# Performance work log

Hardware: AMD Instinct MI355X
Metric: run time of the kernel (lower is better)

The kernel has to match this reference:

```python
import math
import jax, jax.numpy as jnp
import numpy as np

GRID = (256, 256, 256)
K = 9                # kernel_size (already odd)
SIGMA = K / 4.0
PAD = K // 2
CLIP = 0.03


def _gaussian_kernel():
    ax = np.arange(K, dtype=np.float32)
    mean = (K - 1) / 2.0
    g = np.exp(-(((ax - mean) / SIGMA) ** 2) / 2.0) / (SIGMA * math.sqrt(2.0 * math.pi))
    k = g[:, None, None] * g[None, :, None] * g[None, None, :]
    k = k / k.sum()
    return jnp.asarray(k, dtype=jnp.float32).reshape(1, 1, K, K, K)  # OIDHW


def setup_inputs() -> dict:
    key = jax.random.key(0)
    x = jax.random.normal(key, (int(np.prod(GRID)),), dtype=jnp.float32)
    kernel = _gaussian_kernel()
    return {"x": x, "kernel": kernel}


def reference(x, kernel):
    v = x.reshape(1, 1, *GRID)  # [1,1,D,H,W]
    # reflect padding (torch padding_mode='reflect', padding = K//2)
    p = jnp.pad(v, ((0, 0), (0, 0), (PAD, PAD), (PAD, PAD), (PAD, PAD)), mode="reflect")
    # torch Conv3d is cross-correlation; lax conv does not flip kernels either
    out = jax.lax.conv_general_dilated(
        p, kernel,
        window_strides=(1, 1, 1),
        padding="VALID",
        dimension_numbers=("NCDHW", "OIDHW", "NCDHW"),
    )
    # clip: keep smoothed output within +/-CLIP of the original input
    out = jnp.maximum(jnp.minimum(v, out + CLIP), out - CLIP)
    return out.reshape(-1)
```

## Files before the change

kernel.cpp:

```cpp
#include <hip/hip_runtime.h>
#include <hip/hip_fp16.h>
#include <math.h>

#define CLIPV 0.03f

struct W9 { float g[9]; };
struct half4 { __half2 a, b; };

__device__ __forceinline__ int reflect_idx(int i, int n) {
    if (i < 0) i = -i;
    if (i >= n) i = 2 * n - 2 - i;
    return i;
}

__device__ __forceinline__ float4 h4_to_f4(half4 v) {
    const float2 ab = __half22float2(v.a), cd = __half22float2(v.b);
    float4 r; r.x = ab.x; r.y = ab.y; r.z = cd.x; r.w = cd.y; return r;
}
__device__ __forceinline__ half4 f4_to_h4(float4 v) {
    half4 r; r.a = __floats2half2_rn(v.x, v.y); r.b = __floats2half2_rn(v.z, v.w);
    return r;
}

__global__ __launch_bounds__(256, 4) void wh_pass(const float* __restrict__ x,
                                                  __half* __restrict__ t2, W9 wt) {
    const int bid = blockIdx.x;
    const int xcd = bid & 7;
    const int k   = bid >> 3;
    const int z   = xcd * 32 + (k >> 2);
    const int wv  = threadIdx.x >> 6;
    const int h0  = ((k & 3) * 4 + wv) * 16;
    const int L   = threadIdx.x & 63;
    const int w4  = L * 4;
    const bool l0 = (L == 0), l63 = (L == 63);
    const int offL = l0 ? 1 : (w4 - 4);
    const int offR = l63 ? 251 : (w4 + 4);

    const float* plane  = x  + (size_t)z * 65536;
    __half*      oplane = t2 + (size_t)z * 65536;

    float4 ring[9];

    float4 cLf, cCf, cRf, nLf, nCf, nRf;
    {
        const float* r0 = plane + (size_t)reflect_idx(h0 - 4, 256) * 256;
        cLf = *(const float4*)(r0 + offL);
        cCf = *(const float4*)(r0 + w4);
        cRf = *(const float4*)(r0 + offR);
        const float* r1 = plane + (size_t)reflect_idx(h0 - 3, 256) * 256;
        nLf = *(const float4*)(r1 + offL);
        nCf = *(const float4*)(r1 + w4);
        nRf = *(const float4*)(r1 + offR);
    }

    #pragma unroll
    for (int i = 0; i < 24; ++i) {
        float4 mLf, mCf, mRf;
        if (i < 22) {
            const float* row = plane + (size_t)reflect_idx(h0 - 2 + i, 256) * 256;
            mLf = *(const float4*)(row + offL);
            mCf = *(const float4*)(row + w4);
            mRf = *(const float4*)(row + offR);
        }

        float sv[12];
        sv[0] = l0 ? cLf.w : cLf.x;
        sv[1] = l0 ? cLf.z : cLf.y;
        sv[2] = l0 ? cLf.y : cLf.z;
        sv[3] = l0 ? cLf.x : cLf.w;
        sv[4] = cCf.x; sv[5] = cCf.y; sv[6] = cCf.z; sv[7] = cCf.w;
        sv[8]  = l63 ? cRf.w : cRf.x;
        sv[9]  = l63 ? cRf.z : cRf.y;
        sv[10] = l63 ? cRf.y : cRf.z;
        sv[11] = l63 ? cRf.x : cRf.w;

        {
            float a0 = 0.f, a1 = 0.f, a2 = 0.f, a3 = 0.f;
            #pragma unroll
            for (int j = 0; j < 9; ++j) {
                a0 = fmaf(wt.g[j], sv[j],     a0);
                a1 = fmaf(wt.g[j], sv[j + 1], a1);
                a2 = fmaf(wt.g[j], sv[j + 2], a2);
                a3 = fmaf(wt.g[j], sv[j + 3], a3);
            }
            float4 wc; wc.x = a0; wc.y = a1; wc.z = a2; wc.w = a3;
            ring[i % 9] = wc;
        }

        if (i >= 8) {
            float a0 = 0.f, a1 = 0.f, a2 = 0.f, a3 = 0.f;
            #pragma unroll
            for (int j = 0; j < 9; ++j) {
                const float4 v = ring[(i - 8 + j) % 9];
                a0 = fmaf(wt.g[j], v.x, a0);
                a1 = fmaf(wt.g[j], v.y, a1);
                a2 = fmaf(wt.g[j], v.z, a2);
                a3 = fmaf(wt.g[j], v.w, a3);
            }
            float4 o; o.x = a0; o.y = a1; o.z = a2; o.w = a3;
            *(half4*)(oplane + (size_t)(h0 + i - 8) * 256 + w4) = f4_to_h4(o);
        }

        cLf = nLf; cCf = nCf; cRf = nRf;
        nLf = mLf; nCf = mCf; nRf = mRf;
    }
}

__global__ __launch_bounds__(256) void d_clip_pass(const __half* __restrict__ t2,
                                                   const float* __restrict__ x,
                                                   float* __restrict__ out, W9 wt) {
    const int bid   = blockIdx.x;
    const int xcd   = bid & 7;
    const int k     = bid >> 3;
    const int chunk = xcd * 2 + (k & 1);
    const int tile  = k >> 1;
    const int z0    = chunk * 16;
    const size_t c4 = (size_t)tile * 256 + threadIdx.x;

    const half4*  t4 = (const half4*)t2;
    const float4* xp = (const float4*)x;
    float4*       o4 = (float4*)out;

    float4 ring[9];

    half4 cur = t4[(size_t)reflect_idx(z0 - 4, 256) * 16384 + c4];
    half4 nxt = t4[(size_t)reflect_idx(z0 - 3, 256) * 16384 + c4];
    float4 xCur, xNxt;

    #pragma unroll
    for (int i = 0; i < 24; ++i) {
        half4 nn;
        if (i < 22)
            nn = t4[(size_t)reflect_idx(z0 - 2 + i, 256) * 16384 + c4];
        float4 xNew;
        if (i >= 6 && i < 22)
            xNew = xp[(size_t)(z0 + i - 6) * 16384 + c4];

        ring[i % 9] = h4_to_f4(cur);

        if (i >= 8) {
            const int z = z0 + i - 8;
            float a0 = 0.f, a1 = 0.f, a2 = 0.f, a3 = 0.f;
            #pragma unroll
            for (int j = 0; j < 9; ++j) {
                const float4 v = ring[(i - 8 + j) % 9];
                a0 = fmaf(wt.g[j], v.x, a0);
                a1 = fmaf(wt.g[j], v.y, a1);
                a2 = fmaf(wt.g[j], v.z, a2);
                a3 = fmaf(wt.g[j], v.w, a3);
            }
            const float4 xv = xCur;
            float4 r;
            r.x = fmaxf(fminf(xv.x, a0 + CLIPV), a0 - CLIPV);
            r.y = fmaxf(fminf(xv.y, a1 + CLIPV), a1 - CLIPV);
            r.z = fmaxf(fminf(xv.z, a2 + CLIPV), a2 - CLIPV);
            r.w = fmaxf(fminf(xv.w, a3 + CLIPV), a3 - CLIPV);
            o4[(size_t)z * 16384 + c4] = r;
        }

        cur = nxt; nxt = nn;
        xCur = xNxt; xNxt = xNew;
    }
}

extern "C" void kernel_launch(void* const* d_in, const int* in_sizes, int n_in,
                              void* d_out, int out_size, void* d_ws, size_t ws_size,
                              hipStream_t stream) {
    const float* x = (const float*)d_in[0];
    float* out = (float*)d_out;
    __half* t2 = (__half*)d_ws;

    W9 wt;
    {
        double g[9], s = 0.0;
        const double sigma = 9.0 / 4.0;
        for (int i = 0; i < 9; ++i) {
            double tt = (i - 4.0) / sigma;
            g[i] = exp(-0.5 * tt * tt);
            s += g[i];
        }
        for (int i = 0; i < 9; ++i) wt.g[i] = (float)(g[i] / s);
    }

    wh_pass<<<dim3(1024), dim3(256), 0, stream>>>(x, t2, wt);
    d_clip_pass<<<dim3(1024), dim3(256), 0, stream>>>(t2, x, out, wt);
}
```

Measured before the change: 52.75 us.

## Split fused W/H separable pass into separate H and W kernels

After: 76.10 us. +44.3%, slower.

```diff
diff --git a/kernel.cpp b/kernel.cpp
--- a/kernel.cpp
+++ b/kernel.cpp
@@ -22,70 +22,31 @@
     return r;
 }
 
-__global__ __launch_bounds__(256, 4) void wh_pass(const float* __restrict__ x,
-                                                  __half* __restrict__ t2, W9 wt) {
+__global__ __launch_bounds__(256) void h_pass(const float* __restrict__ x,
+                                              __half* __restrict__ t1, W9 wt) {
     const int bid = blockIdx.x;
     const int xcd = bid & 7;
     const int k   = bid >> 3;
     const int z   = xcd * 32 + (k >> 2);
     const int wv  = threadIdx.x >> 6;
     const int h0  = ((k & 3) * 4 + wv) * 16;
-    const int L   = threadIdx.x & 63;
-    const int w4  = L * 4;
-    const bool l0 = (L == 0), l63 = (L == 63);
-    const int offL = l0 ? 1 : (w4 - 4);
-    const int offR = l63 ? 251 : (w4 + 4);
+    const int w4  = (threadIdx.x & 63) * 4;
 
     const float* plane  = x  + (size_t)z * 65536;
-    __half*      oplane = t2 + (size_t)z * 65536;
+    __half*      oplane = t1 + (size_t)z * 65536;
 
     float4 ring[9];
 
-    float4 cLf, cCf, cRf, nLf, nCf, nRf;
-    {
-        const float* r0 = plane + (size_t)reflect_idx(h0 - 4, 256) * 256;
-        cLf = *(const float4*)(r0 + offL);
-        cCf = *(const float4*)(r0 + w4);
-        cRf = *(const float4*)(r0 + offR);
-        const float* r1 = plane + (size_t)reflect_idx(h0 - 3, 256) * 256;
-        nLf = *(const float4*)(r1 + offL);
-        nCf = *(const float4*)(r1 + w4);
-        nRf = *(const float4*)(r1 + offR);
-    }
+    float4 cur = *(const float4*)(plane + (size_t)reflect_idx(h0 - 4, 256) * 256 + w4);
+    float4 nxt = *(const float4*)(plane + (size_t)reflect_idx(h0 - 3, 256) * 256 + w4);
 
     #pragma unroll
     for (int i = 0; i < 24; ++i) {
-        float4 mLf, mCf, mRf;
-        if (i < 22) {
-            const float* row = plane + (size_t)reflect_idx(h0 - 2 + i, 256) * 256;
-            mLf = *(const float4*)(row + offL);
-            mCf = *(const float4*)(row + w4);
-            mRf = *(const float4*)(row + offR);
-        }
-
-        float sv[12];
-        sv[0] = l0 ? cLf.w : cLf.x;
-        sv[1] = l0 ? cLf.z : cLf.y;
-        sv[2] = l0 ? cLf.y : cLf.z;
-        sv[3] = l0 ? cLf.x : cLf.w;
-        sv[4] = cCf.x; sv[5] = cCf.y; sv[6] = cCf.z; sv[7] = cCf.w;
-        sv[8]  = l63 ? cRf.w : cRf.x;
-        sv[9]  = l63 ? cRf.z : cRf.y;
-        sv[10] = l63 ? cRf.y : cRf.z;
-        sv[11] = l63 ? cRf.x : cRf.w;
-
-        {
-            float a0 = 0.f, a1 = 0.f, a2 = 0.f, a3 = 0.f;
-            #pragma unroll
-            for (int j = 0; j < 9; ++j) {
-                a0 = fmaf(wt.g[j], sv[j],     a0);
-                a1 = fmaf(wt.g[j], sv[j + 1], a1);
-                a2 = fmaf(wt.g[j], sv[j + 2], a2);
-                a3 = fmaf(wt.g[j], sv[j + 3], a3);
-            }
-            float4 wc; wc.x = a0; wc.y = a1; wc.z = a2; wc.w = a3;
-            ring[i % 9] = wc;
-        }
+        float4 nn;
+        if (i < 22)
+            nn = *(const float4*)(plane + (size_t)reflect_idx(h0 - 2 + i, 256) * 256 + w4);
+
+        ring[i % 9] = cur;
 
         if (i >= 8) {
             float a0 = 0.f, a1 = 0.f, a2 = 0.f, a3 = 0.f;
@@ -101,8 +62,74 @@
             *(half4*)(oplane + (size_t)(h0 + i - 8) * 256 + w4) = f4_to_h4(o);
         }
 
-        cLf = nLf; cCf = nCf; cRf = nRf;
-        nLf = mLf; nCf = mCf; nRf = mRf;
+        cur = nxt; nxt = nn;
+    }
+}
+
+__global__ __launch_bounds__(256) void wt_pass(const __half* __restrict__ t1,
+                                               __half* __restrict__ t2, W9 wt) {
+    const int bid  = blockIdx.x;
+    const int xcd  = bid & 7;
+    const int k    = bid >> 3;
+    const int z    = xcd * 32 + (k >> 2);
+    const int band = (k & 3) * 64;
+    const int wv   = threadIdx.x >> 6;
+    const int c0   = wv * 64;
+    const int L    = threadIdx.x & 63;
+    const int r    = band + L;
+
+    const __half* row  = t1 + (size_t)z * 65536 + (size_t)r * 256;
+    __half*       orow = t2 + (size_t)z * 65536 + (size_t)r * 256;
+
+    const bool wL = (c0 == 0), wR = (c0 == 192);
+
+    float4 w0, w1, w2;
+    half4 p1, p2;
+    if (wL) {
+        w1 = h4_to_f4(*(const half4*)(row + 0));
+        w2 = h4_to_f4(*(const half4*)(row + 4));
+        w0.x = w2.x; w0.y = w1.w; w0.z = w1.z; w0.w = w1.y;
+    } else {
+        w0 = h4_to_f4(*(const half4*)(row + c0 - 4));
+        w1 = h4_to_f4(*(const half4*)(row + c0));
+        w2 = h4_to_f4(*(const half4*)(row + c0 + 4));
+    }
+    p1 = *(const half4*)(row + c0 + 8);
+    p2 = *(const half4*)(row + c0 + 12);
+
+    #pragma unroll
+    for (int t = 0; t < 16; ++t) {
+        const int c = c0 + 4 * t;
+
+        half4 pNew;
+        if (t <= 12) {
+            int cl = c0 + 16 + 4 * t;
+            if (wR && cl > 252) cl = 252;
+            pNew = *(const half4*)(row + cl);
+        }
+
+        const float sv[12] = {w0.x, w0.y, w0.z, w0.w,
+                              w1.x, w1.y, w1.z, w1.w,
+                              w2.x, w2.y, w2.z, w2.w};
+        float a0 = 0.f, a1 = 0.f, a2 = 0.f, a3 = 0.f;
+        #pragma unroll
+        for (int j = 0; j < 9; ++j) {
+            a0 = fmaf(wt.g[j], sv[j],     a0);
+            a1 = fmaf(wt.g[j], sv[j + 1], a1);
+            a2 = fmaf(wt.g[j], sv[j + 2], a2);
+            a3 = fmaf(wt.g[j], sv[j + 3], a3);
+        }
+        float4 o; o.x = a0; o.y = a1; o.z = a2; o.w = a3;
+        *(half4*)(orow + c) = f4_to_h4(o);
+
+        if (t < 15) {
+            w0 = w1; w1 = w2; w2 = h4_to_f4(p1);
+            p1 = p2; p2 = pNew;
+            if (wR && t == 14) {
+                float4 fx; fx.x = w1.z; fx.y = w1.y; fx.z = w1.x; fx.w = w0.w;
+                w2 = fx;
+            }
+        }
     }
 }
 
@@ -168,7 +195,8 @@
                               hipStream_t stream) {
     const float* x = (const float*)d_in[0];
     float* out = (float*)d_out;
-    __half* t2 = (__half*)d_ws;
+    __half* t1 = (__half*)d_ws;
+    __half* t2 = t1 + 16777216;
 
     W9 wt;
     {
@@ -182,6 +210,7 @@
         for (int i = 0; i < 9; ++i) wt.g[i] = (float)(g[i] / s);
     }
 
-    wh_pass<<<dim3(1024), dim3(256), 0, stream>>>(x, t2, wt);
+    h_pass<<<dim3(1024), dim3(256), 0, stream>>>(x, t1, wt);
+    wt_pass<<<dim3(1024), dim3(256), 0, stream>>>(t1, t2, wt);
     d_clip_pass<<<dim3(1024), dim3(256), 0, stream>>>(t2, x, out, wt);
 }
```

## Swap H/W order in first pass, staging H-filtered rows in LDS

Applied to the files above, without the earlier changes.

New measurement: 53.67 us. No clear change (+1.7%).

```diff
diff --git a/kernel.cpp b/kernel.cpp
--- a/kernel.cpp
+++ b/kernel.cpp
@@ -22,87 +22,87 @@
     return r;
 }
 
-__global__ __launch_bounds__(256, 4) void wh_pass(const float* __restrict__ x,
-                                                  __half* __restrict__ t2, W9 wt) {
+__global__ __launch_bounds__(256) void wh_pass(const float* __restrict__ x,
+                                               __half* __restrict__ t2, W9 wt) {
+    __shared__ __half tile[64][264];
+
     const int bid = blockIdx.x;
     const int xcd = bid & 7;
     const int k   = bid >> 3;
     const int z   = xcd * 32 + (k >> 2);
+    const int rb  = (k & 3) * 64;
     const int wv  = threadIdx.x >> 6;
-    const int h0  = ((k & 3) * 4 + wv) * 16;
+    const int h0  = rb + wv * 16;
     const int L   = threadIdx.x & 63;
     const int w4  = L * 4;
+
+    const float* plane = x + (size_t)z * 65536;
+
+    {
+        float4 ring[9];
+        float4 cur = *(const float4*)(plane + (size_t)reflect_idx(h0 - 4, 256) * 256 + w4);
+        float4 nxt = *(const float4*)(plane + (size_t)reflect_idx(h0 - 3, 256) * 256 + w4);
+
+        #pragma unroll
+        for (int i = 0; i < 24; ++i) {
+            float4 nn;
+            if (i < 22)
+                nn = *(const float4*)(plane + (size_t)reflect_idx(h0 - 2 + i, 256) * 256 + w4);
+
+            ring[i % 9] = cur;
+
+            if (i >= 8) {
+                float a0 = 0.f, a1 = 0.f, a2 = 0.f, a3 = 0.f;
+                #pragma unroll
+                for (int j = 0; j < 9; ++j) {
+                    const float4 v = ring[(i - 8 + j) % 9];
+                    a0 = fmaf(wt.g[j], v.x, a0);
+                    a1 = fmaf(wt.g[j], v.y, a1);
+                    a2 = fmaf(wt.g[j], v.z, a2);
+                    a3 = fmaf(wt.g[j], v.w, a3);
+                }
+                float4 o; o.x = a0; o.y = a1; o.z = a2; o.w = a3;
+                *(half4*)&tile[wv * 16 + (i - 8)][w4] = f4_to_h4(o);
+            }
+
+            cur = nxt; nxt = nn;
+        }
+    }
+    __syncthreads();
+
+    __half* oplane = t2 + (size_t)z * 65536 + (size_t)rb * 256;
     const bool l0 = (L == 0), l63 = (L == 63);
-    const int offL = l0 ? 1 : (w4 - 4);
-    const int offR = l63 ? 251 : (w4 + 4);
-
-    const float* plane  = x  + (size_t)z * 65536;
-    __half*      oplane = t2 + (size_t)z * 65536;
-
-    float4 ring[9];
-
-    float4 cLf, cCf, cRf, nLf, nCf, nRf;
-    {
-        const float* r0 = plane + (size_t)reflect_idx(h0 - 4, 256) * 256;
-        cLf = *(const float4*)(r0 + offL);
-        cCf = *(const float4*)(r0 + w4);
-        cRf = *(const float4*)(r0 + offR);
-        const float* r1 = plane + (size_t)reflect_idx(h0 - 3, 256) * 256;
-        nLf = *(const float4*)(r1 + offL);
-        nCf = *(const float4*)(r1 + w4);
-        nRf = *(const float4*)(r1 + offR);
-    }
+    const int offA = l0  ? w4 : (w4 - 4);
+    const int offC = l63 ? w4 : (w4 + 4);
 
     #pragma unroll
-    for (int i = 0; i < 24; ++i) {
-        float4 mLf, mCf, mRf;
-        if (i < 22) {
-            const float* row = plane + (size_t)reflect_idx(h0 - 2 + i, 256) * 256;
-            mLf = *(const float4*)(row + offL);
-            mCf = *(const float4*)(row + w4);
-            mRf = *(const float4*)(row + offR);
-        }
+    for (int s = 0; s < 16; ++s) {
+        const int r = wv * 16 + s;
+        const float4 A = h4_to_f4(*(const half4*)&tile[r][offA]);
+        const float4 B = h4_to_f4(*(const half4*)&tile[r][w4]);
+        const float4 C = h4_to_f4(*(const half4*)&tile[r][offC]);
 
         float sv[12];
-        sv[0] = l0 ? cLf.w : cLf.x;
-        sv[1] = l0 ? cLf.z : cLf.y;
-        sv[2] = l0 ? cLf.y : cLf.z;
-        sv[3] = l0 ? cLf.x : cLf.w;
-        sv[4] = cCf.x; sv[5] = cCf.y; sv[6] = cCf.z; sv[7] = cCf.w;
-        sv[8]  = l63 ? cRf.w : cRf.x;
-        sv[9]  = l63 ? cRf.z : cRf.y;
-        sv[10] = l63 ? cRf.y : cRf.z;
-        sv[11] = l63 ? cRf.x : cRf.w;
+        sv[0] = l0 ? C.x : A.x;
+        sv[1] = l0 ? B.w : A.y;
+        sv[2] = l0 ? B.z : A.z;
+        sv[3] = l0 ? B.y : A.w;
+        sv[4] = B.x; sv[5] = B.y; sv[6] = B.z; sv[7] = B.w;
+        sv[8]  = l63 ? B.z : C.x;
+        sv[9]  = l63 ? B.y : C.y;
+        sv[10] = l63 ? B.x : C.z;
+        sv[11] = l63 ? A.w : C.w;
 
-        {
-            float a0 = 0.f, a1 = 0.f, a2 = 0.f, a3 = 0.f;
-            #pragma unroll
-            for (int j = 0; j < 9; ++j) {
-                a0 = fmaf(wt.g[j], sv[j],     a0);
-                a1 = fmaf(wt.g[j], sv[j + 1], a1);
-                a2 = fmaf(wt.g[j], sv[j + 2], a2);
-                a3 = fmaf(wt.g[j], sv[j + 3], a3);
-            }
-            float4 wc; wc.x = a0; wc.y = a1; wc.z = a2; wc.w = a3;
-            ring[i % 9] = wc;
+        float a0 = 0.f, a1 = 0.f, a2 = 0.f, a3 = 0.f;
+        #pragma unroll
+        for (int j = 0; j < 9; ++j) {
+            a0 = fmaf(wt.g[j], sv[j],     a0);
+            a1 = fmaf(wt.g[j], sv[j + 1], a1);
+            a2 = fmaf(wt.g[j], sv[j + 2], a2);
+            a3 = fmaf(wt.g[j], sv[j + 3], a3);
         }
-
-        if (i >= 8) {
-            float a0 = 0.f, a1 = 0.f, a2 = 0.f, a3 = 0.f;
-            #pragma unroll
-            for (int j = 0; j < 9; ++j) {
-                const float4 v = ring[(i - 8 + j) % 9];
-                a0 = fmaf(wt.g[j], v.x, a0);
-                a1 = fmaf(wt.g[j], v.y, a1);
-                a2 = fmaf(wt.g[j], v.z, a2);
-                a3 = fmaf(wt.g[j], v.w, a3);
-            }
-            float4 o; o.x = a0; o.y = a1; o.z = a2; o.w = a3;
-            *(half4*)(oplane + (size_t)(h0 + i - 8) * 256 + w4) = f4_to_h4(o);
-        }
-
-        cLf = nLf; cCf = nCf; cRf = nRf;
-        nLf = mLf; nCf = mCf; nRf = mRf;
+        float4 o; o.x = a0; o.y = a1; o.z = a2; o.w = a3;
+        *(half4*)(oplane + (size_t)r * 256 + w4) = f4_to_h4(o);
     }
 }
 
```
